# Optimization experiments

Hardware: AMD Instinct MI355X
Metric: run time of the kernel (lower is better)

Reference implementation:

```python
import jax, jax.numpy as jnp
import numpy as np

K = 256      # embedding size k
STATE = 128  # latent state size
IN = 64      # external input size
OBS = 64     # observation size
L = 512      # sequence length (time-major)
B = 256      # batch size


def _glorot(key, shape):
    return jax.random.normal(key, shape, dtype=jnp.float32) / float(np.sqrt(shape[0]))


def setup_inputs():
    key = jax.random.key(0)
    ks = jax.random.split(key, 12)
    p = {}
    p["external_input_seq"] = jax.random.normal(ks[0], (L, B, IN), dtype=jnp.float32)
    p["observations_seq"] = jax.random.normal(ks[1], (L, B, OBS), dtype=jnp.float32)
    p["eps"] = jax.random.normal(ks[2], (L, B, STATE), dtype=jnp.float32)  # reparam noise
    # PreProcess: Linear + tanh
    p["Wu"] = _glorot(ks[3], (IN, K)); p["bu"] = jnp.zeros((K,), jnp.float32)
    p["Wx"] = _glorot(ks[4], (OBS, K)); p["bx"] = jnp.zeros((K,), jnp.float32)
    # input_rnn: vanilla tanh RNN, 1 layer, k -> k
    p["W_ih"] = _glorot(ks[5], (K, K)); p["b_ih"] = jnp.zeros((K,), jnp.float32)
    p["W_hh"] = _glorot(ks[6], (K, K)); p["b_hh"] = jnp.zeros((K,), jnp.float32)
    # posterior_a_layer: MLP(2k, k, k, 1) = Linear -> tanh -> Linear
    p["Wa1"] = _glorot(ks[7], (2 * K, K)); p["ba1"] = jnp.zeros((K,), jnp.float32)
    p["Wa2"] = _glorot(ks[8], (K, K)); p["ba2"] = jnp.zeros((K,), jnp.float32)

    def dblock_params(k1, in_dim, hid, out):
        kk = jax.random.split(k1, 4)
        return (_glorot(kk[0], (in_dim, hid)), jnp.zeros((hid,), jnp.float32),
                _glorot(kk[1], (in_dim, hid)), jnp.zeros((hid,), jnp.float32),
                _glorot(kk[2], (hid, out)), jnp.zeros((out,), jnp.float32),
                _glorot(kk[3], (hid, out)), jnp.zeros((out,), jnp.float32))

    names = ["f1_W", "f1_b", "f2_W", "f2_b", "mu_W", "mu_b", "ls_W", "ls_b"]
    for pref, kk in (("post_", ks[9]), ("prior_", ks[10])):
        vals = dblock_params(kk, STATE + K, 2 * K, STATE)
        for n, v in zip(names, vals):
            p[pref + n] = v
    return p


def _dblock(x, f1_W, f1_b, f2_W, f2_b, mu_W, mu_b, ls_W, ls_b):
    # TD-VAE DBlock: gated hidden, then mu / logsigma heads
    t = jnp.tanh(x @ f1_W + f1_b) * jax.nn.sigmoid(x @ f2_W + f2_b)
    return t @ mu_W + mu_b, t @ ls_W + ls_b


def reference(external_input_seq, observations_seq, eps, Wu, bu, Wx, bx,
              W_ih, b_ih, W_hh, b_hh, Wa1, ba1, Wa2, ba2,
              post_f1_W, post_f1_b, post_f2_W, post_f2_b, post_mu_W, post_mu_b, post_ls_W, post_ls_b,
              prior_f1_W, prior_f1_b, prior_f2_W, prior_f2_b, prior_mu_W, prior_mu_b, prior_ls_W, prior_ls_b):
    batch = external_input_seq.shape[1]
    u_emb = jnp.tanh(external_input_seq @ Wu + bu)   # [L,B,K]
    x_emb = jnp.tanh(observations_seq @ Wx + bx)     # [L,B,K]

    # input_rnn (tanh RNN) over time, d0 = 0 (memory_state=None)
    def rnn_step(d, x):
        d_new = jnp.tanh(x @ W_ih + b_ih + d @ W_hh + b_hh)
        return d_new, d_new
    d0 = jnp.zeros((batch, W_hh.shape[0]), dtype=u_emb.dtype)
    dn, d_seq = jax.lax.scan(rnn_step, d0, u_emb)    # dn [B,K], d_seq [L,B,K]

    # posterior_a_layer: pointwise MLP; flip(0) then flip(0) is a no-op for a pointwise map
    ad = jnp.concatenate([d_seq, x_emb], axis=-1)    # [L,B,2K]
    a_seq = jnp.tanh(ad @ Wa1 + ba1) @ Wa2 + ba2     # [L,B,K]

    state_size = post_mu_W.shape[1]
    z0 = jnp.zeros((batch, state_size), dtype=u_emb.dtype)

    def step(z_prev, inp):
        a_t, d_t, e_t = inp
        mean_res, logsigma = _dblock(jnp.concatenate([z_prev, a_t], axis=-1),
                                     post_f1_W, post_f1_b, post_f2_W, post_f2_b,
                                     post_mu_W, post_mu_b, post_ls_W, post_ls_b)
        prior_mean = _dblock(jnp.concatenate([z_prev, d_t], axis=-1),
                             prior_f1_W, prior_f1_b, prior_f2_W, prior_f2_b,
                             prior_mu_W, prior_mu_b, prior_ls_W, prior_ls_b)[0]
        mu = prior_mean + mean_res
        # cov = diag(exp(logsigma)) -> std = exp(0.5*logsigma); reparameterized sample
        z_new = mu + jnp.exp(0.5 * logsigma) * e_t
        return z_new, (mu, logsigma)

    zn, (state_mu, state_logsigma) = jax.lax.scan(step, z0, (a_seq, d_seq, eps))
    return state_mu, state_logsigma, dn, zn
```

## Files before the change

kernel.cpp:

```cpp
#include <hip/hip_runtime.h>

#define LSEQ 512
#define BATCH 256
#define KDIM 256
#define STATE 128

using f32x4  = __attribute__((ext_vector_type(4))) float;
using short8 = __attribute__((ext_vector_type(8))) short;

__device__ __forceinline__ float bf2f(unsigned short u){
  return __uint_as_float(((unsigned int)u) << 16);
}
__device__ __forceinline__ unsigned short f2bf(float f){
  unsigned int u = __float_as_uint(f);
  u += 0x7FFFu + ((u >> 16) & 1u);
  return (unsigned short)(u >> 16);
}
__device__ __forceinline__ float fast_tanh(float x){
  float ax = fabsf(x);
  float e  = __expf(2.0f * ax);
  float t  = 1.0f - 2.0f / (e + 1.0f);
  return copysignf(t, x);
}
__device__ __forceinline__ float fast_sig(float x){
  return 1.0f / (1.0f + __expf(-x));
}
__device__ __forceinline__ f32x4 mfma16(short8 a, short8 b, f32x4 c){
  return __builtin_amdgcn_mfma_f32_16x16x32_bf16(a, b, c, 0, 0, 0);
}

__device__ __forceinline__ int swz128 (int b){ return b ^ ((((b >> 7) & 7) << 4)); }
__device__ __forceinline__ int swz256 (int b){ return b ^ ((((b >> 8) & 7) << 4)); }
__device__ __forceinline__ int swz512 (int b){ return b ^ ((((b >> 9) & 7) << 4)); }

__device__ __forceinline__ void mb_store(float* p, float v){
  __hip_atomic_store(p, v, __ATOMIC_RELAXED, __HIP_MEMORY_SCOPE_AGENT);
}
__device__ __forceinline__ float mb_load(const float* p){
  return __hip_atomic_load(p, __ATOMIC_RELAXED, __HIP_MEMORY_SCOPE_AGENT);
}

struct WDesc { const float* src; unsigned short* dst; int K, N, ld, rowoff, coloff; };
struct WDescs { WDesc d[24]; };

__global__ __launch_bounds__(256,4) void convert_weights(WDescs ds){
  WDesc w = ds.d[blockIdx.y];
  int total = w.K * w.N;
  int idx = blockIdx.x * 256 + threadIdx.x;
  if (idx < total){
    int n = idx / w.K;
    int k = idx - n * w.K;
    w.dst[idx] = f2bf(w.src[(size_t)(w.rowoff + k) * w.ld + w.coloff + n]);
  }
}

__global__ __launch_bounds__(256,1) void init_flags(int* flags){
  flags[blockIdx.x * 256 + threadIdx.x] = 0;
}

struct GArg {
  const void* A; const unsigned short* Bt; const float* bias;
  unsigned short* C; int lda, ldc, coff, K, act, a_f32;
};
struct GArgs { GArg g[4]; };

__global__ __launch_bounds__(256,2) void gemm_multi(GArgs args){
  GArg ga = args.g[blockIdx.z];
  __shared__ __align__(16) unsigned short lsA[128*64];
  __shared__ __align__(16) unsigned short lsB[128*64];
  const int tid  = threadIdx.x;
  const int wave = tid >> 6, lane = tid & 63;
  const int col_l = lane & 15, rgrp = lane >> 4;
  const int m0 = blockIdx.x * 128, n0 = blockIdx.y * 128;
  const int wm = (wave >> 1) * 64, wn = (wave & 1) * 64;

  f32x4 acc[4][4];
  const f32x4 z4 = {0.f,0.f,0.f,0.f};
  #pragma unroll
  for (int i=0;i<4;i++){ acc[i][0]=z4; acc[i][1]=z4; acc[i][2]=z4; acc[i][3]=z4; }

  const int srow = tid >> 1;
  const int sbe  = (tid & 1) * 32;

  for (int k0 = 0; k0 < ga.K; k0 += 64){
    uint4 av[4], bv[4];
    if (ga.a_f32){
      const float* Ap = (const float*)ga.A + (size_t)(m0 + srow) * ga.lda + k0 + sbe;
      uint4 fv[8];
      #pragma unroll
      for (int i=0;i<8;i++) fv[i] = *(const uint4*)((const char*)Ap + i*16);
      #pragma unroll
      for (int i=0;i<4;i++){
        const float* f = (const float*)&fv[i*2];
        uint4 o;
        o.x = (unsigned)f2bf(f[0]) | ((unsigned)f2bf(f[1]) << 16);
        o.y = (unsigned)f2bf(f[2]) | ((unsigned)f2bf(f[3]) << 16);
        o.z = (unsigned)f2bf(f[4]) | ((unsigned)f2bf(f[5]) << 16);
        o.w = (unsigned)f2bf(f[6]) | ((unsigned)f2bf(f[7]) << 16);
        av[i] = o;
      }
    } else {
      const unsigned short* Ap = (const unsigned short*)ga.A + (size_t)(m0 + srow) * ga.lda + k0 + sbe;
      #pragma unroll
      for (int i=0;i<4;i++) av[i] = *(const uint4*)((const char*)Ap + i*16);
    }
    const unsigned short* Bp = ga.Bt + (size_t)(n0 + srow) * ga.K + k0 + sbe;
    #pragma unroll
    for (int i=0;i<4;i++) bv[i] = *(const uint4*)((const char*)Bp + i*16);

    __syncthreads();
    #pragma unroll
    for (int i=0;i<4;i++){
      *(uint4*)((char*)lsA + swz128(srow*128 + sbe*2 + i*16)) = av[i];
      *(uint4*)((char*)lsB + swz128(srow*128 + sbe*2 + i*16)) = bv[i];
    }
    __syncthreads();
    #pragma unroll
    for (int kk=0; kk<2; kk++){
      short8 af[4], bfr[4];
      #pragma unroll
      for (int mt=0; mt<4; mt++)
        af[mt] = *(const short8*)((const char*)lsA + swz128((wm + mt*16 + col_l)*128 + kk*64 + rgrp*16));
      #pragma unroll
      for (int nt=0; nt<4; nt++)
        bfr[nt] = *(const short8*)((const char*)lsB + swz128((wn + nt*16 + col_l)*128 + kk*64 + rgrp*16));
      #pragma unroll
      for (int mt=0; mt<4; mt++)
        #pragma unroll
        for (int nt=0; nt<4; nt++)
          acc[mt][nt] = mfma16(af[mt], bfr[nt], acc[mt][nt]);
    }
  }
  #pragma unroll
  for (int nt=0; nt<4; nt++){
    int col = n0 + wn + nt*16 + col_l;
    float bb = ga.bias ? ga.bias[col] : 0.0f;
    #pragma unroll
    for (int mt=0; mt<4; mt++){
      #pragma unroll
      for (int r=0; r<4; r++){
        int row = m0 + wm + mt*16 + rgrp*4 + r;
        float v = acc[mt][nt][r] + bb;
        if (ga.act == 1) v = fast_tanh(v);
        ga.C[(size_t)row * ga.ldc + ga.coff + col] = f2bf(v);
      }
    }
  }
}

__global__ __launch_bounds__(256,1) void rnn_chunk(
    const unsigned short* __restrict__ rnn_in,
    const unsigned short* __restrict__ Whh_t,
    const float* __restrict__ b_hh,
    unsigned short* __restrict__ cat_d,
    float* __restrict__ dn_out,
    unsigned short* __restrict__ d_state,
    int t0, int nsteps)
{
  __shared__ __align__(16) unsigned short dls[16*256];
  const int tid = threadIdx.x, wave = tid >> 6, lane = tid & 63;
  const int col_l = lane & 15, rgrp = lane >> 4;
  const int brow0 = blockIdx.x * 16;
  const int ncol = wave * 64;

  short8 bfr[4][8];
  #pragma unroll
  for (int nt=0; nt<4; nt++){
    const unsigned short* bp = Whh_t + (size_t)(ncol + nt*16 + col_l) * 256;
    #pragma unroll
    for (int kk=0; kk<8; kk++)
      bfr[nt][kk] = *(const short8*)(bp + kk*32 + rgrp*8);
  }
  float bias[4];
  #pragma unroll
  for (int nt=0; nt<4; nt++) bias[nt] = b_hh[ncol + nt*16 + col_l];

  if (t0 == 0){
    for (int i = tid; i < 16*256; i += 256){
      int row = i >> 8, col = i & 255;
      *(unsigned short*)((char*)dls + swz512(row*512 + col*2)) = 0;
    }
  } else {
    const unsigned short* ds = d_state + (size_t)brow0 * 256;
    for (int i = tid; i < 16*256; i += 256){
      int row = i >> 8, col = i & 255;
      *(unsigned short*)((char*)dls + swz512(row*512 + col*2)) = ds[row*256 + col];
    }
  }
  __syncthreads();

  for (int tl=0; tl<nsteps; tl++){
    unsigned short rv[4][4];
    const unsigned short* rp = rnn_in + (size_t)(tl*BATCH + brow0) * 256;
    #pragma unroll
    for (int nt=0; nt<4; nt++)
      #pragma unroll
      for (int r=0; r<4; r++)
        rv[nt][r] = rp[(size_t)(rgrp*4 + r)*256 + ncol + nt*16 + col_l];

    f32x4 acc[4];
    const f32x4 z4 = {0.f,0.f,0.f,0.f};
    acc[0]=z4; acc[1]=z4; acc[2]=z4; acc[3]=z4;
    #pragma unroll
    for (int kk=0; kk<8; kk++){
      short8 af = *(const short8*)((const char*)dls + swz512((lane & 15)*512 + kk*64 + rgrp*16));
      #pragma unroll
      for (int nt=0; nt<4; nt++)
        acc[nt] = mfma16(af, bfr[nt][kk], acc[nt]);
    }
    __syncthreads();
    #pragma unroll
    for (int nt=0; nt<4; nt++){
      #pragma unroll
      for (int r=0; r<4; r++){
        float h = acc[nt][r] + bf2f(rv[nt][r]) + bias[nt];
        float d = fast_tanh(h);
        int row = rgrp*4 + r, col = ncol + nt*16 + col_l;
        unsigned short db = f2bf(d);
        *(unsigned short*)((char*)dls + swz512(row*512 + col*2)) = db;
        cat_d[(size_t)(tl*BATCH + brow0 + row)*512 + col] = db;
        if (t0 + tl == LSEQ-1) dn_out[(size_t)(brow0 + row)*256 + col] = d;
      }
    }
    __syncthreads();
  }
  unsigned short* dso = d_state + (size_t)brow0 * 256;
  for (int i = tid; i < 16*256; i += 256){
    int row = i >> 8, col = i & 255;
    dso[row*256 + col] = *(const unsigned short*)((const char*)dls + swz512(row*512 + col*2));
  }
}

__global__ __launch_bounds__(512) void zrec_mb(
    const unsigned short* __restrict__ preP1, const unsigned short* __restrict__ preP2,
    const unsigned short* __restrict__ preQ1, const unsigned short* __restrict__ preQ2,
    const unsigned short* __restrict__ Wzz,
    const unsigned short* __restrict__ W2,
    const float* __restrict__ pmub, const float* __restrict__ plsb, const float* __restrict__ qmub,
    const float* __restrict__ eps,
    float* __restrict__ out_mu, float* __restrict__ out_ls, float* __restrict__ out_zn,
    unsigned short* __restrict__ z_state,
    float* __restrict__ mb, int* __restrict__ flags,
    int t0, int nsteps)
{
  __shared__ __align__(16) unsigned short zls[16*128];
  __shared__ __align__(16) unsigned short tls[16*256];
  const int tid = threadIdx.x, wave = tid >> 6, lane = tid & 63;
  const int col_l = lane & 15, rgrp = lane >> 4;
  const int bid = blockIdx.x;
  const int c   = (bid >> 3) & 3;
  const int g   = (bid & 7) + ((bid >> 5) << 3);
  const int brow0 = g * 16;
  const int NT2 = (c < 2) ? 2 : 1;

  const unsigned short* pA = (c < 2) ? preP1 : preQ1;
  const unsigned short* pB = (c < 2) ? preP2 : preQ2;
  const int cb = (c & 1) * 256;

  short8 w1[2][2][4];
  {
    const unsigned short* wz = Wzz + (size_t)c * 65536;
    #pragma unroll
    for (int m=0; m<2; m++)
      #pragma unroll
      for (int nt=0; nt<2; nt++){
        int n = wave*32 + nt*16 + col_l;
        #pragma unroll
        for (int kk=0; kk<4; kk++)
          w1[m][nt][kk] = *(const short8*)(wz + (size_t)(m*256 + n)*128 + kk*32 + rgrp*8);
      }
  }
  short8 w2r[2][8];
  {
    const unsigned short* wp = W2 + (size_t)c * 65536;
    #pragma unroll
    for (int nt=0; nt<2; nt++){
      if (nt < NT2){
        int ccol = wave*(16*((c<2)?2:1)) + nt*16;
        int mat = (c < 2) ? (ccol >> 7) : 0;
        int n   = (ccol & 127) + col_l;
        #pragma unroll
        for (int kk=0; kk<8; kk++)
          w2r[nt][kk] = *(const short8*)(wp + (size_t)(mat*128 + n)*256 + kk*32 + rgrp*8);
      }
    }
  }
  const int zcol = wave*16 + col_l;
  const float bp = pmub[zcol], bl = plsb[zcol], bq = qmub[zcol];
  int* const myflag = flags + (g*4 + c)*32;

  if (t0 == 0){
    for (int i = tid; i < 16*128; i += 512){
      int row = i >> 7, col = i & 127;
      *(unsigned short*)((char*)zls + swz256(row*256 + col*2)) = 0;
    }
  } else {
    const unsigned short* zs = z_state + (size_t)brow0 * 128;
    for (int i = tid; i < 16*128; i += 512){
      int row = i >> 7, col = i & 127;
      *(unsigned short*)((char*)zls + swz256(row*256 + col*2)) = zs[row*128 + col];
    }
  }
  __syncthreads();

  auto LD_PRE = [&](int tl, unsigned short (&pa_)[2][4], unsigned short (&pb_)[2][4]){
    const unsigned short* bA = pA + ((size_t)tl*BATCH + brow0)*512 + cb;
    const unsigned short* bB = pB + ((size_t)tl*BATCH + brow0)*512 + cb;
    #pragma unroll
    for (int nt=0; nt<2; nt++)
      #pragma unroll
      for (int r=0; r<4; r++){
        int row = rgrp*4 + r, col = wave*32 + nt*16 + col_l;
        pa_[nt][r] = bA[(size_t)row*512 + col];
        pb_[nt][r] = bB[(size_t)row*512 + col];
      }
  };

  unsigned short pa0[2][4], pb0[2][4], pa1[2][4], pb1[2][4];
  LD_PRE(0, pa0, pb0);

  const f32x4 z4 = {0.f,0.f,0.f,0.f};
  for (int tl=0; tl<nsteps; ++tl){
    float er[4];
    #pragma unroll
    for (int r=0; r<4; r++){
      size_t grow = (size_t)(t0+tl)*BATCH + brow0 + rgrp*4 + r;
      er[r] = eps[grow*STATE + zcol];
    }
    int nx = (tl+1 < nsteps) ? tl+1 : tl;
    LD_PRE(nx, pa1, pb1);

    short8 af1[4];
    #pragma unroll
    for (int kk=0; kk<4; kk++)
      af1[kk] = *(const short8*)((const char*)zls + swz256((lane & 15)*256 + kk*64 + rgrp*16));
    f32x4 a1[2][2];
    a1[0][0]=z4; a1[0][1]=z4; a1[1][0]=z4; a1[1][1]=z4;
    #pragma unroll
    for (int kk=0; kk<4; kk++)
      #pragma unroll
      for (int m=0; m<2; m++)
        #pragma unroll
        for (int nt=0; nt<2; nt++)
          a1[m][nt] = mfma16(af1[kk], w1[m][nt][kk], a1[m][nt]);

    #pragma unroll
    for (int nt=0; nt<2; nt++)
      #pragma unroll
      for (int r=0; r<4; r++){
        float h1 = a1[0][nt][r] + bf2f(pa0[nt][r]);
        float h2 = a1[1][nt][r] + bf2f(pb0[nt][r]);
        float tv = fast_tanh(h1) * fast_sig(h2);
        int row = rgrp*4 + r, tcol = wave*32 + nt*16 + col_l;
        *(unsigned short*)((char*)tls + swz512(row*512 + tcol*2)) = f2bf(tv);
      }
    __syncthreads();

    f32x4 a2[2];
    a2[0]=z4; a2[1]=z4;
    #pragma unroll
    for (int kk=0; kk<8; kk++){
      short8 af2 = *(const short8*)((const char*)tls + swz512((lane & 15)*512 + kk*64 + rgrp*16));
      #pragma unroll
      for (int nt=0; nt<2; nt++)
        if (nt < NT2) a2[nt] = mfma16(af2, w2r[nt][kk], a2[nt]);
    }
    float* slot = mb + ((size_t)(g*2 + (tl & 1))*4 + c)*4096;
    #pragma unroll
    for (int nt=0; nt<2; nt++)
      if (nt < NT2){
        #pragma unroll
        for (int r=0; r<4; r++){
          int ccol = wave*(16*((c<2)?2:1)) + nt*16 + col_l;
          mb_store(&slot[(rgrp*4 + r)*256 + ccol], a2[nt][r]);
        }
      }
    __syncthreads();
    if (tid == 0)
      __hip_atomic_fetch_add(myflag, 1, __ATOMIC_RELAXED, __HIP_MEMORY_SCOPE_AGENT);

    if (wave >= 1 && wave <= 3 && lane == 0){
      int p = (c + wave) & 3;
      int* pf = flags + (g*4 + p)*32;
      while (__hip_atomic_load(pf, __ATOMIC_RELAXED, __HIP_MEMORY_SCOPE_AGENT) < tl+1)
        __builtin_amdgcn_s_sleep(1);
    }
    __syncthreads();

    const float* mbb = mb + (size_t)(g*2 + (tl & 1))*4*4096;
    #pragma unroll
    for (int r=0; r<4; r++){
      int row = rgrp*4 + r;
      const float* r0 = mbb + row*256;
      float mup = mb_load(&r0[zcol])          + mb_load(&r0[4096 + zcol]);
      float lsp = mb_load(&r0[128 + zcol])    + mb_load(&r0[4096 + 128 + zcol]);
      float muq = mb_load(&r0[2*4096 + zcol]) + mb_load(&r0[3*4096 + zcol]);
      float mu  = (muq + bq) + (mup + bp);
      float ls  = lsp + bl;
      float z   = mu + __expf(0.5f * ls) * er[r];
      *(unsigned short*)((char*)zls + swz256(row*256 + zcol*2)) = f2bf(z);
      if (c == 0){
        size_t grow = (size_t)(t0+tl)*BATCH + brow0 + row;
        out_mu[grow*STATE + zcol] = mu;
        out_ls[grow*STATE + zcol] = ls;
        if (t0 + tl == LSEQ-1) out_zn[((size_t)(brow0 + row))*STATE + zcol] = z;
      }
    }
    __syncthreads();

    #pragma unroll
    for (int nt=0; nt<2; nt++)
      #pragma unroll
      for (int r=0; r<4; r++){ pa0[nt][r] = pa1[nt][r]; pb0[nt][r] = pb1[nt][r]; }
  }

  if (c == 0){
    unsigned short* zso = z_state + (size_t)brow0 * 128;
    for (int i = tid; i < 16*128; i += 512){
      int row = i >> 7, col = i & 127;
      zso[row*128 + col] = *(const unsigned short*)((const char*)zls + swz256(row*256 + col*2));
    }
  }
}

extern "C" void kernel_launch(void* const* d_in, const int* in_sizes, int n_in,
                              void* d_out, int out_size, void* d_ws, size_t ws_size,
                              hipStream_t stream)
{
  const float* ext = (const float*)d_in[0];
  const float* obs = (const float*)d_in[1];
  const float* eps = (const float*)d_in[2];
  const float* Wu  = (const float*)d_in[3];
  const float* bu  = (const float*)d_in[4];
  const float* Wx  = (const float*)d_in[5];
  const float* bx  = (const float*)d_in[6];
  const float* W_ih= (const float*)d_in[7];
  const float* b_ih= (const float*)d_in[8];
  const float* W_hh= (const float*)d_in[9];
  const float* b_hh= (const float*)d_in[10];
  const float* Wa1 = (const float*)d_in[11];
  const float* ba1 = (const float*)d_in[12];
  const float* Wa2 = (const float*)d_in[13];
  const float* ba2 = (const float*)d_in[14];
  const float* pf1W= (const float*)d_in[15]; const float* pf1b = (const float*)d_in[16];
  const float* pf2W= (const float*)d_in[17]; const float* pf2b = (const float*)d_in[18];
  const float* pmuW= (const float*)d_in[19]; const float* pmub = (const float*)d_in[20];
  const float* plsW= (const float*)d_in[21]; const float* plsb = (const float*)d_in[22];
  const float* qf1W= (const float*)d_in[23]; const float* qf1b = (const float*)d_in[24];
  const float* qf2W= (const float*)d_in[25]; const float* qf2b = (const float*)d_in[26];
  const float* qmuW= (const float*)d_in[27]; const float* qmub = (const float*)d_in[28];

  int NC = 0;
  const int cands[7] = {1,2,4,8,16,32,64};
  size_t rows = 0;
  for (int ci=0; ci<7; ci++){
    size_t r = (size_t)(LSEQ/cands[ci])*BATCH;
    size_t elems = 2700000 + r*3072;
    if (elems * 2 <= ws_size){ NC = cands[ci]; rows = r; break; }
  }
  if (!NC) return;
  const int nsteps = LSEQ/NC;
  const int gx = (int)(rows/128);

  unsigned short* ws = (unsigned short*)d_ws;
  size_t off = 0;
  auto alloc = [&](size_t elems){
    unsigned short* p = ws + off;
    off += (elems + 127) & ~(size_t)127;
    return p;
  };

  unsigned short* Wu_t  = alloc(64*256);
  unsigned short* Wx_t  = alloc(64*256);
  unsigned short* Wih_t = alloc(256*256);
  unsigned short* Whh_t = alloc(256*256);
  unsigned short* Wa1_t = alloc(512*256);
  unsigned short* Wa2_t = alloc(256*256);
  unsigned short* f1a_p = alloc(256*512);
  unsigned short* f2a_p = alloc(256*512);
  unsigned short* f1a_q = alloc(256*512);
  unsigned short* f2a_q = alloc(256*512);
  unsigned short* Wzz   = alloc(4*2*256*128);
  unsigned short* W2z   = alloc(4*2*128*256);
  unsigned short* d_state = alloc(256*256);
  unsigned short* z_state = alloc(256*128);
  float* mbx  = (float*)alloc(2*16*2*4*4096);
  int*   flg  = (int*)alloc(2*2048);
  unsigned short* bufA  = alloc(rows*256);
  unsigned short* bufB  = alloc(rows*256);
  unsigned short* bufC  = alloc(rows*512);
  unsigned short* preP1 = alloc(rows*512);
  unsigned short* preP2 = alloc(rows*512);
  unsigned short* preQ1 = alloc(rows*512);
  unsigned short* preQ2 = alloc(rows*512);
  if (off * sizeof(unsigned short) > ws_size) return;

  float* out_mu = (float*)d_out;
  float* out_ls = out_mu + (size_t)LSEQ*BATCH*STATE;
  float* out_dn = out_ls + (size_t)LSEQ*BATCH*STATE;
  float* out_zn = out_dn + (size_t)BATCH*KDIM;

  WDescs wd;
  int wi = 0;
  auto add = [&](const float* s, unsigned short* d, int Kk, int Nn, int ld, int ro, int co){
    wd.d[wi].src = s; wd.d[wi].dst = d; wd.d[wi].K = Kk; wd.d[wi].N = Nn;
    wd.d[wi].ld = ld; wd.d[wi].rowoff = ro; wd.d[wi].coloff = co; wi++;
  };
  add(Wu,   Wu_t,  64, 256, 256, 0, 0);
  add(Wx,   Wx_t,  64, 256, 256, 0, 0);
  add(W_ih, Wih_t, 256, 256, 256, 0, 0);
  add(W_hh, Whh_t, 256, 256, 256, 0, 0);
  add(Wa1,  Wa1_t, 512, 256, 256, 0, 0);
  add(Wa2,  Wa2_t, 256, 256, 256, 0, 0);
  add(pf1W, f1a_p, 256, 512, 512, 128, 0);
  add(pf2W, f2a_p, 256, 512, 512, 128, 0);
  add(qf1W, f1a_q, 256, 512, 512, 128, 0);
  add(qf2W, f2a_q, 256, 512, 512, 128, 0);
  for (int c=0; c<4; c++){
    const float* s1 = (c < 2) ? pf1W : qf1W;
    const float* s2 = (c < 2) ? pf2W : qf2W;
    add(s1, Wzz + (size_t)(c*2+0)*32768, 128, 256, 512, 0, (c&1)*256);
    add(s2, Wzz + (size_t)(c*2+1)*32768, 128, 256, 512, 0, (c&1)*256);
  }
  add(pmuW, W2z + (size_t)(0*2+0)*32768, 256, 128, 128, 0,   0);
  add(plsW, W2z + (size_t)(0*2+1)*32768, 256, 128, 128, 0,   0);
  add(pmuW, W2z + (size_t)(1*2+0)*32768, 256, 128, 128, 256, 0);
  add(plsW, W2z + (size_t)(1*2+1)*32768, 256, 128, 128, 256, 0);
  add(qmuW, W2z + (size_t)(2*2+0)*32768, 256, 128, 128, 0,   0);
  add(qmuW, W2z + (size_t)(3*2+0)*32768, 256, 128, 128, 256, 0);

  convert_weights<<<dim3(512,24), 256, 0, stream>>>(wd);

  for (int c=0; c<NC; ++c){
    const int t0 = c * nsteps;
    const size_t row0 = (size_t)t0 * BATCH;

    GArgs e{};
    e.g[0] = GArg{ext + row0*64, Wu_t, bu, bufA, 64, 256, 0,   64, 1, 1};
    e.g[1] = GArg{obs + row0*64, Wx_t, bx, bufC, 64, 512, 256, 64, 1, 1};
    gemm_multi<<<dim3(gx,2,2), 256, 0, stream>>>(e);

    GArgs rn{};
    rn.g[0] = GArg{bufA, Wih_t, b_ih, bufB, 256, 256, 0, 256, 0, 0};
    gemm_multi<<<dim3(gx,2,1), 256, 0, stream>>>(rn);

    rnn_chunk<<<16, 256, 0, stream>>>(bufB, Whh_t, b_hh, bufC, out_dn, d_state, t0, nsteps);

    GArgs a1{};
    a1.g[0] = GArg{bufC, Wa1_t, ba1, bufA, 512, 256, 0, 512, 1, 0};
    gemm_multi<<<dim3(gx,2,1), 256, 0, stream>>>(a1);

    GArgs a2{};
    a2.g[0] = GArg{bufA, Wa2_t, ba2, bufB, 256, 256, 0, 256, 0, 0};
    gemm_multi<<<dim3(gx,2,1), 256, 0, stream>>>(a2);

    GArgs pr{};
    pr.g[0] = GArg{bufB, f1a_p, pf1b, preP1, 256, 512, 0, 256, 0, 0};
    pr.g[1] = GArg{bufB, f2a_p, pf2b, preP2, 256, 512, 0, 256, 0, 0};
    pr.g[2] = GArg{bufC, f1a_q, qf1b, preQ1, 512, 512, 0, 256, 0, 0};
    pr.g[3] = GArg{bufC, f2a_q, qf2b, preQ2, 512, 512, 0, 256, 0, 0};
    gemm_multi<<<dim3(gx,4,4), 256, 0, stream>>>(pr);

    init_flags<<<8, 256, 0, stream>>>(flg);
    zrec_mb<<<64, 512, 0, stream>>>(preP1, preP2, preQ1, preQ2, Wzz, W2z,
                                    pmub, plsb, qmub, eps, out_mu, out_ls, out_zn,
                                    z_state, mbx, flg, t0, nsteps);
  }
}
```

Measured before the change: 3.979 ms.

## Stage bf16 partials through LDS and exchange with vector cache-bypassing stores

The per-step cross-block exchange in the z recurrence now packs each block's partial head outputs into LDS as bf16. It then writes them to the mailbox with one 128-bit or 64-bit store per thread using sc0 sc1, replacing many scalar fp32 atomic stores. Flags become monotonic stores with a running target, so flags are reset once instead of before every chunk. Readers fetch packed bf16 via vectorized loads, and eps and output accesses become f32x4. The four pre-activation GEMM outputs are also merged into two wider buffers, so one gemm_multi launch with a dual-bias epilogue produces them. Exchanging partials in bf16 lowers precision, and the inline-asm cache-control coherence is subtle.

```diff
diff --git a/kernel.cpp b/kernel.cpp
--- a/kernel.cpp
+++ b/kernel.cpp
@@ -7,6 +7,8 @@
 
 using f32x4  = __attribute__((ext_vector_type(4))) float;
 using short8 = __attribute__((ext_vector_type(8))) short;
+using u32x2  = __attribute__((ext_vector_type(2))) unsigned int;
+using u32x4  = __attribute__((ext_vector_type(4))) unsigned int;
 
 __device__ __forceinline__ float bf2f(unsigned short u){
   return __uint_as_float(((unsigned int)u) << 16);
@@ -33,11 +35,21 @@
 __device__ __forceinline__ int swz256 (int b){ return b ^ ((((b >> 8) & 7) << 4)); }
 __device__ __forceinline__ int swz512 (int b){ return b ^ ((((b >> 9) & 7) << 4)); }
 
-__device__ __forceinline__ void mb_store(float* p, float v){
-  __hip_atomic_store(p, v, __ATOMIC_RELAXED, __HIP_MEMORY_SCOPE_AGENT);
-}
-__device__ __forceinline__ float mb_load(const float* p){
-  return __hip_atomic_load(p, __ATOMIC_RELAXED, __HIP_MEMORY_SCOPE_AGENT);
+__device__ __forceinline__ void st_b128_ic(void* p, u32x4 v){
+  asm volatile("global_store_dwordx4 %0, %1, off sc0 sc1" :: "v"(p), "v"(v) : "memory");
+}
+__device__ __forceinline__ void st_b64_ic(void* p, u32x2 v){
+  asm volatile("global_store_dwordx2 %0, %1, off sc0 sc1" :: "v"(p), "v"(v) : "memory");
+}
+#define LD2_IC(dst, p) asm volatile("global_load_dwordx2 %0, %1, off sc0 sc1" : "=v"(dst) : "v"(p) : "memory")
+
+__device__ __forceinline__ f32x4 cvt4(u32x2 q){
+  f32x4 r;
+  r[0] = __uint_as_float(q[0] << 16);
+  r[1] = __uint_as_float(q[0] & 0xFFFF0000u);
+  r[2] = __uint_as_float(q[1] << 16);
+  r[3] = __uint_as_float(q[1] & 0xFFFF0000u);
+  return r;
 }
 
 struct WDesc { const float* src; unsigned short* dst; int K, N, ld, rowoff, coloff; };
@@ -59,7 +71,7 @@
 }
 
 struct GArg {
-  const void* A; const unsigned short* Bt; const float* bias;
+  const void* A; const unsigned short* Bt; const float* bias; const float* bias2;
   unsigned short* C; int lda, ldc, coff, K, act, a_f32;
 };
 struct GArgs { GArg g[4]; };
@@ -134,7 +146,8 @@
   #pragma unroll
   for (int nt=0; nt<4; nt++){
     int col = n0 + wn + nt*16 + col_l;
-    float bb = ga.bias ? ga.bias[col] : 0.0f;
+    const float* bsrc = (col < 512) ? ga.bias : ga.bias2;
+    float bb = bsrc ? bsrc[col & 511] : 0.0f;
     #pragma unroll
     for (int mt=0; mt<4; mt++){
       #pragma unroll
@@ -231,17 +244,16 @@
   }
 }
 
-__global__ __launch_bounds__(512) void zrec_mb(
-    const unsigned short* __restrict__ preP1, const unsigned short* __restrict__ preP2,
-    const unsigned short* __restrict__ preQ1, const unsigned short* __restrict__ preQ2,
+__global__ __launch_bounds__(512,1) void zrec_mb(
+    const unsigned short* __restrict__ preP, const unsigned short* __restrict__ preQ,
     const unsigned short* __restrict__ Wzz,
     const unsigned short* __restrict__ W2,
     const float* __restrict__ pmub, const float* __restrict__ plsb, const float* __restrict__ qmub,
     const float* __restrict__ eps,
     float* __restrict__ out_mu, float* __restrict__ out_ls, float* __restrict__ out_zn,
     unsigned short* __restrict__ z_state,
-    float* __restrict__ mb, int* __restrict__ flags,
-    int t0, int nsteps)
+    unsigned short* __restrict__ mb, int* __restrict__ flags,
+    int t0, int nsteps, int fbase)
 {
   __shared__ __align__(16) unsigned short zls[16*128];
   __shared__ __align__(16) unsigned short tls[16*256];
@@ -253,8 +265,7 @@
   const int brow0 = g * 16;
   const int NT2 = (c < 2) ? 2 : 1;
 
-  const unsigned short* pA = (c < 2) ? preP1 : preQ1;
-  const unsigned short* pB = (c < 2) ? preP2 : preQ2;
+  const unsigned short* pre = (c < 2) ? preP : preQ;
   const int cb = (c & 1) * 256;
 
   short8 w1[2][2][4];
@@ -285,8 +296,6 @@
       }
     }
   }
-  const int zcol = wave*16 + col_l;
-  const float bp = pmub[zcol], bl = plsb[zcol], bq = qmub[zcol];
   int* const myflag = flags + (g*4 + c)*32;
 
   if (t0 == 0){
@@ -304,29 +313,30 @@
   __syncthreads();
 
   auto LD_PRE = [&](int tl, unsigned short (&pa_)[2][4], unsigned short (&pb_)[2][4]){
-    const unsigned short* bA = pA + ((size_t)tl*BATCH + brow0)*512 + cb;
-    const unsigned short* bB = pB + ((size_t)tl*BATCH + brow0)*512 + cb;
+    const unsigned short* bA = pre + ((size_t)tl*BATCH + brow0)*1024 + cb;
     #pragma unroll
     for (int nt=0; nt<2; nt++)
       #pragma unroll
       for (int r=0; r<4; r++){
         int row = rgrp*4 + r, col = wave*32 + nt*16 + col_l;
-        pa_[nt][r] = bA[(size_t)row*512 + col];
-        pb_[nt][r] = bB[(size_t)row*512 + col];
+        pa_[nt][r] = bA[(size_t)row*1024 + col];
+        pb_[nt][r] = bA[(size_t)row*1024 + 512 + col];
       }
   };
 
+  const int rrow = tid >> 5;
+  const int rc0  = (tid & 31) * 4;
+  const f32x4 bp4 = *(const f32x4*)(pmub + rc0);
+  const f32x4 bl4 = *(const f32x4*)(plsb + rc0);
+  const f32x4 bq4 = *(const f32x4*)(qmub + rc0);
+
   unsigned short pa0[2][4], pb0[2][4], pa1[2][4], pb1[2][4];
   LD_PRE(0, pa0, pb0);
 
   const f32x4 z4 = {0.f,0.f,0.f,0.f};
   for (int tl=0; tl<nsteps; ++tl){
-    float er[4];
-    #pragma unroll
-    for (int r=0; r<4; r++){
-      size_t grow = (size_t)(t0+tl)*BATCH + brow0 + rgrp*4 + r;
-      er[r] = eps[grow*STATE + zcol];
-    }
+    size_t growr = (size_t)(t0+tl)*BATCH + brow0 + rrow;
+    f32x4 er = *(const f32x4*)(eps + growr*STATE + rc0);
     int nx = (tl+1 < nsteps) ? tl+1 : tl;
     LD_PRE(nx, pa1, pb1);
 
@@ -365,46 +375,74 @@
       for (int nt=0; nt<2; nt++)
         if (nt < NT2) a2[nt] = mfma16(af2, w2r[nt][kk], a2[nt]);
     }
-    float* slot = mb + ((size_t)(g*2 + (tl & 1))*4 + c)*4096;
-    #pragma unroll
-    for (int nt=0; nt<2; nt++)
-      if (nt < NT2){
+    __syncthreads();
+
+    if (c < 2){
+      #pragma unroll
+      for (int nt=0; nt<2; nt++)
         #pragma unroll
-        for (int r=0; r<4; r++){
-          int ccol = wave*(16*((c<2)?2:1)) + nt*16 + col_l;
-          mb_store(&slot[(rgrp*4 + r)*256 + ccol], a2[nt][r]);
-        }
-      }
-    __syncthreads();
+        for (int r=0; r<4; r++)
+          tls[(rgrp*4 + r)*256 + wave*32 + nt*16 + col_l] = f2bf(a2[nt][r]);
+    } else {
+      #pragma unroll
+      for (int r=0; r<4; r++)
+        tls[(rgrp*4 + r)*128 + wave*16 + col_l] = f2bf(a2[0][r]);
+    }
+    __syncthreads();
+
+    unsigned short* slot = mb + (size_t)((g*2 + (tl & 1))*4 + c)*4096;
+    if (c < 2){
+      u32x4 v = *(const u32x4*)((const char*)tls + tid*16);
+      st_b128_ic(slot + tid*8, v);
+    } else {
+      u32x2 v = *(const u32x2*)((const char*)tls + tid*8);
+      st_b64_ic(slot + tid*4, v);
+    }
+    asm volatile("s_waitcnt vmcnt(0)" ::: "memory");
+    __syncthreads();
+    const int target = fbase + tl + 1;
     if (tid == 0)
-      __hip_atomic_fetch_add(myflag, 1, __ATOMIC_RELAXED, __HIP_MEMORY_SCOPE_AGENT);
-
-    if (wave >= 1 && wave <= 3 && lane == 0){
-      int p = (c + wave) & 3;
-      int* pf = flags + (g*4 + p)*32;
-      while (__hip_atomic_load(pf, __ATOMIC_RELAXED, __HIP_MEMORY_SCOPE_AGENT) < tl+1)
+      __hip_atomic_store(myflag, target, __ATOMIC_RELAXED, __HIP_MEMORY_SCOPE_AGENT);
+
+    if (wave == 7 && lane < 3){
+      const int* pf = flags + (g*4 + ((c + 1 + lane) & 3))*32;
+      while (__hip_atomic_load(pf, __ATOMIC_RELAXED, __HIP_MEMORY_SCOPE_AGENT) < target)
         __builtin_amdgcn_s_sleep(1);
     }
     __syncthreads();
 
-    const float* mbb = mb + (size_t)(g*2 + (tl & 1))*4*4096;
-    #pragma unroll
-    for (int r=0; r<4; r++){
-      int row = rgrp*4 + r;
-      const float* r0 = mbb + row*256;
-      float mup = mb_load(&r0[zcol])          + mb_load(&r0[4096 + zcol]);
-      float lsp = mb_load(&r0[128 + zcol])    + mb_load(&r0[4096 + 128 + zcol]);
-      float muq = mb_load(&r0[2*4096 + zcol]) + mb_load(&r0[3*4096 + zcol]);
-      float mu  = (muq + bq) + (mup + bp);
-      float ls  = lsp + bl;
-      float z   = mu + __expf(0.5f * ls) * er[r];
-      *(unsigned short*)((char*)zls + swz256(row*256 + zcol*2)) = f2bf(z);
-      if (c == 0){
-        size_t grow = (size_t)(t0+tl)*BATCH + brow0 + row;
-        out_mu[grow*STATE + zcol] = mu;
-        out_ls[grow*STATE + zcol] = ls;
-        if (t0 + tl == LSEQ-1) out_zn[((size_t)(brow0 + row))*STATE + zcol] = z;
-      }
+    const unsigned short* mbb = mb + (size_t)((g*2 + (tl & 1))*4)*4096;
+    const unsigned short* s0 = mbb;
+    const unsigned short* s1 = mbb + 4096;
+    const unsigned short* s2 = mbb + 8192;
+    const unsigned short* s3 = mbb + 12288;
+    u32x2 q0,q1,q2,q3,q4,q5;
+    LD2_IC(q0, s0 + rrow*256 + rc0);
+    LD2_IC(q1, s1 + rrow*256 + rc0);
+    LD2_IC(q2, s0 + rrow*256 + 128 + rc0);
+    LD2_IC(q3, s1 + rrow*256 + 128 + rc0);
+    LD2_IC(q4, s2 + rrow*128 + rc0);
+    LD2_IC(q5, s3 + rrow*128 + rc0);
+    asm volatile("s_waitcnt vmcnt(0)" ::: "memory");
+    __builtin_amdgcn_sched_barrier(0);
+
+    f32x4 mup = cvt4(q0) + cvt4(q1);
+    f32x4 lsv = cvt4(q2) + cvt4(q3) + bl4;
+    f32x4 muq = cvt4(q4) + cvt4(q5);
+    f32x4 muv = (muq + bq4) + (mup + bp4);
+    f32x4 zv;
+    #pragma unroll
+    for (int i=0; i<4; i++) zv[i] = muv[i] + __expf(0.5f * lsv[i]) * er[i];
+
+    unsigned int lo = (unsigned)f2bf(zv[0]) | ((unsigned)f2bf(zv[1]) << 16);
+    unsigned int hi = (unsigned)f2bf(zv[2]) | ((unsigned)f2bf(zv[3]) << 16);
+    uint2 zp; zp.x = lo; zp.y = hi;
+    *(uint2*)((char*)zls + swz256(rrow*256 + rc0*2)) = zp;
+    if (c == 0){
+      *(f32x4*)(out_mu + growr*STATE + rc0) = muv;
+      *(f32x4*)(out_ls + growr*STATE + rc0) = lsv;
+      if (t0 + tl == LSEQ-1)
+        *(f32x4*)(out_zn + ((size_t)(brow0 + rrow))*STATE + rc0) = zv;
     }
     __syncthreads();
 
@@ -476,23 +514,19 @@
   unsigned short* Whh_t = alloc(256*256);
   unsigned short* Wa1_t = alloc(512*256);
   unsigned short* Wa2_t = alloc(256*256);
-  unsigned short* f1a_p = alloc(256*512);
-  unsigned short* f2a_p = alloc(256*512);
-  unsigned short* f1a_q = alloc(256*512);
-  unsigned short* f2a_q = alloc(256*512);
+  unsigned short* fAp   = alloc(1024*256);
+  unsigned short* fAq   = alloc(1024*256);
   unsigned short* Wzz   = alloc(4*2*256*128);
   unsigned short* W2z   = alloc(4*2*128*256);
   unsigned short* d_state = alloc(256*256);
   unsigned short* z_state = alloc(256*128);
-  float* mbx  = (float*)alloc(2*16*2*4*4096);
-  int*   flg  = (int*)alloc(2*2048);
+  unsigned short* mbx  = alloc(16*2*4*4096);
+  int*   flg  = (int*)alloc(4096);
   unsigned short* bufA  = alloc(rows*256);
   unsigned short* bufB  = alloc(rows*256);
   unsigned short* bufC  = alloc(rows*512);
-  unsigned short* preP1 = alloc(rows*512);
-  unsigned short* preP2 = alloc(rows*512);
-  unsigned short* preQ1 = alloc(rows*512);
-  unsigned short* preQ2 = alloc(rows*512);
+  unsigned short* preP  = alloc(rows*1024);
+  unsigned short* preQ  = alloc(rows*1024);
   if (off * sizeof(unsigned short) > ws_size) return;
 
   float* out_mu = (float*)d_out;
@@ -512,10 +546,10 @@
   add(W_hh, Whh_t, 256, 256, 256, 0, 0);
   add(Wa1,  Wa1_t, 512, 256, 256, 0, 0);
   add(Wa2,  Wa2_t, 256, 256, 256, 0, 0);
-  add(pf1W, f1a_p, 256, 512, 512, 128, 0);
-  add(pf2W, f2a_p, 256, 512, 512, 128, 0);
-  add(qf1W, f1a_q, 256, 512, 512, 128, 0);
-  add(qf2W, f2a_q, 256, 512, 512, 128, 0);
+  add(pf1W, fAp,            256, 512, 512, 128, 0);
+  add(pf2W, fAp + 512*256,  256, 512, 512, 128, 0);
+  add(qf1W, fAq,            256, 512, 512, 128, 0);
+  add(qf2W, fAq + 512*256,  256, 512, 512, 128, 0);
   for (int c=0; c<4; c++){
     const float* s1 = (c < 2) ? pf1W : qf1W;
     const float* s2 = (c < 2) ? pf2W : qf2W;
@@ -530,40 +564,38 @@
   add(qmuW, W2z + (size_t)(3*2+0)*32768, 256, 128, 128, 256, 0);
 
   convert_weights<<<dim3(512,24), 256, 0, stream>>>(wd);
+  init_flags<<<8, 256, 0, stream>>>(flg);
 
   for (int c=0; c<NC; ++c){
     const int t0 = c * nsteps;
     const size_t row0 = (size_t)t0 * BATCH;
 
     GArgs e{};
-    e.g[0] = GArg{ext + row0*64, Wu_t, bu, bufA, 64, 256, 0,   64, 1, 1};
-    e.g[1] = GArg{obs + row0*64, Wx_t, bx, bufC, 64, 512, 256, 64, 1, 1};
+    e.g[0] = GArg{ext + row0*64, Wu_t, bu, bu, bufA, 64, 256, 0,   64, 1, 1};
+    e.g[1] = GArg{obs + row0*64, Wx_t, bx, bx, bufC, 64, 512, 256, 64, 1, 1};
     gemm_multi<<<dim3(gx,2,2), 256, 0, stream>>>(e);
 
     GArgs rn{};
-    rn.g[0] = GArg{bufA, Wih_t, b_ih, bufB, 256, 256, 0, 256, 0, 0};
+    rn.g[0] = GArg{bufA, Wih_t, b_ih, b_ih, bufB, 256, 256, 0, 256, 0, 0};
     gemm_multi<<<dim3(gx,2,1), 256, 0, stream>>>(rn);
 
     rnn_chunk<<<16, 256, 0, stream>>>(bufB, Whh_t, b_hh, bufC, out_dn, d_state, t0, nsteps);
 
     GArgs a1{};
-    a1.g[0] = GArg{bufC, Wa1_t, ba1, bufA, 512, 256, 0, 512, 1, 0};
+    a1.g[0] = GArg{bufC, Wa1_t, ba1, ba1, bufA, 512, 256, 0, 512, 1, 0};
     gemm_multi<<<dim3(gx,2,1), 256, 0, stream>>>(a1);
 
     GArgs a2{};
-    a2.g[0] = GArg{bufA, Wa2_t, ba2, bufB, 256, 256, 0, 256, 0, 0};
+    a2.g[0] = GArg{bufA, Wa2_t, ba2, ba2, bufB, 256, 256, 0, 256, 0, 0};
     gemm_multi<<<dim3(gx,2,1), 256, 0, stream>>>(a2);
 
     GArgs pr{};
-    pr.g[0] = GArg{bufB, f1a_p, pf1b, preP1, 256, 512, 0, 256, 0, 0};
-    pr.g[1] = GArg{bufB, f2a_p, pf2b, preP2, 256, 512, 0, 256, 0, 0};
-    pr.g[2] = GArg{bufC, f1a_q, qf1b, preQ1, 512, 512, 0, 256, 0, 0};
-    pr.g[3] = GArg{bufC, f2a_q, qf2b, preQ2, 512, 512, 0, 256, 0, 0};
-    gemm_multi<<<dim3(gx,4,4), 256, 0, stream>>>(pr);
-
-    init_flags<<<8, 256, 0, stream>>>(flg);
-    zrec_mb<<<64, 512, 0, stream>>>(preP1, preP2, preQ1, preQ2, Wzz, W2z,
+    pr.g[0] = GArg{bufB, fAp, pf1b, pf2b, preP, 256, 1024, 0, 256, 0, 0};
+    pr.g[1] = GArg{bufC, fAq, qf1b, qf2b, preQ, 512, 1024, 0, 256, 0, 0};
+    gemm_multi<<<dim3(gx,8,2), 256, 0, stream>>>(pr);
+
+    zrec_mb<<<64, 512, 0, stream>>>(preP, preQ, Wzz, W2z,
                                     pmub, plsb, qmub, eps, out_mu, out_ls, out_zn,
-                                    z_state, mbx, flg, t0, nsteps);
-  }
-}
+                                    z_state, mbx, flg, t0, nsteps, c*nsteps);
+  }
+}
```

Result: no change. 3.902 ms (-1.9%).
